# Performance work log

Hardware: AMD Instinct MI355X
Metric: run time of the kernel (lower is better)

Reference implementation:

```python
import jax, jax.numpy as jnp
import numpy as np

N = 10000       # nodes
E = 320000      # edges (avg degree 32)
F_IN = 128      # node_in_fts
F_OUT = 128     # node_out_fts
H = 4           # num_heads_node
E_IN = 64       # edge_in_fts
HOPS = 3        # nr_of_hops
SLOPE = 0.2     # LeakyReLU negative slope (GAT default)


def setup_inputs() -> dict:
    key = jax.random.key(0)
    ks = jax.random.split(key, 10)
    s = 0.05
    return {
        "node_fts": jax.random.normal(ks[0], (N, F_IN), dtype=jnp.float32),
        "edge_fts": jax.random.normal(ks[1], (E, E_IN), dtype=jnp.float32),
        "edges": jax.random.randint(ks[2], (2, E), 0, N),
        # per-hop GATConv params (all hops share dims, stacked on axis 0)
        "Ws": jax.random.normal(ks[3], (HOPS, F_IN, H * F_OUT), dtype=jnp.float32) * s,
        "Wes": jax.random.normal(ks[4], (HOPS, E_IN, H * F_OUT), dtype=jnp.float32) * s,
        "a_src": jax.random.normal(ks[5], (HOPS, H, F_OUT), dtype=jnp.float32) * s,
        "a_dst": jax.random.normal(ks[6], (HOPS, H, F_OUT), dtype=jnp.float32) * s,
        "a_edge": jax.random.normal(ks[7], (HOPS, H, F_OUT), dtype=jnp.float32) * s,
        # gated residual params
        "W_prior": jax.random.normal(ks[8], (F_OUT, F_OUT), dtype=jnp.float32) * s,
        "W_curr": jax.random.normal(ks[9], (F_OUT, F_OUT), dtype=jnp.float32) * s,
    }


def _gat_conv(x, edge_fts, src, dst, W, We, asrc, adst, aedge):
    # dense projections: [N,H,F_OUT] and [E,H,F_OUT]
    h = (x @ W).reshape(-1, H, F_OUT)
    he = (edge_fts @ We).reshape(-1, H, F_OUT)
    h_src = h[src]                                   # [E,H,F_OUT] gather
    # per-edge attention logits [E,H]
    alpha = (h_src * asrc).sum(-1) + (h[dst] * adst).sum(-1) + (he * aedge).sum(-1)
    alpha = jax.nn.leaky_relu(alpha, SLOPE)
    # segment softmax over incoming edges of each destination node
    amax = jnp.full((N, H), -jnp.inf, dtype=alpha.dtype).at[dst].max(alpha)
    w = jnp.exp(alpha - amax[dst])                   # [E,H]
    denom = jax.ops.segment_sum(w, dst, num_segments=N) + 1e-16  # [N,H]
    msg = w[:, :, None] * h_src                      # [E,H,F_OUT]
    out = jax.ops.segment_sum(msg, dst, num_segments=N) / denom[:, :, None]
    return out.mean(axis=1)                          # mean head aggregation -> [N,F_OUT]


def reference(node_fts, edge_fts, edges, Ws, Wes, a_src, a_dst, a_edge, W_prior, W_curr):
    src, dst = edges[0], edges[1]
    x = node_fts
    prior = None
    for i in range(HOPS):
        curr = _gat_conv(x, edge_fts, src, dst, Ws[i], Wes[i], a_src[i], a_dst[i], a_edge[i])
        if prior is None:
            x = curr
        else:
            gate = jax.nn.sigmoid(prior @ W_prior + curr @ W_curr)
            x = gate * curr + (1.0 - gate) * prior
        prior = x
    return x
```

## Files before the change

### kernel.cpp

```cpp
#include <hip/hip_runtime.h>
#include <hip/hip_fp16.h>

#define N_NODES 10000
#define E_EDGES 320000
#define NH 4
#define HOPS 3
#define WMAX 128

typedef _Float16 f16x8 __attribute__((ext_vector_type(8)));
typedef _Float16 f16x4 __attribute__((ext_vector_type(4)));
typedef float    f32x4 __attribute__((ext_vector_type(4)));

__global__ void k_count(const int* __restrict__ dst, int* __restrict__ counts){
  int e = blockIdx.x*256 + threadIdx.x;
  if(e < E_EDGES) atomicAdd(&counts[dst[e]], 1);
}

__global__ __launch_bounds__(1024) void k_scan(const int* __restrict__ counts,
                                               int* __restrict__ row_ptr, int* __restrict__ fillp){
  __shared__ int sm[1024];
  int t = threadIdx.x;
  const int CH = 10;
  int base = t*CH;
  int loc[CH]; int sum = 0;
  #pragma unroll
  for(int i=0;i<CH;i++){
    int v = (base+i < N_NODES) ? counts[base+i] : 0;
    loc[i] = sum; sum += v;
  }
  sm[t] = sum; __syncthreads();
  for(int off=1; off<1024; off<<=1){
    int add = (t>=off) ? sm[t-off] : 0;
    __syncthreads();
    sm[t] += add;
    __syncthreads();
  }
  int excl = (t>0) ? sm[t-1] : 0;
  #pragma unroll
  for(int i=0;i<CH;i++){
    int n = base+i;
    if(n < N_NODES){
      int e = excl + loc[i];
      row_ptr[n] = e;
      fillp[n]   = e;
    }
  }
  if(t==1023) row_ptr[N_NODES] = sm[1023];
}

__global__ void k_fill(const int* __restrict__ src, const int* __restrict__ dst,
                       int* __restrict__ fillp, int* __restrict__ csr_eid, int* __restrict__ sorted_src){
  int e = blockIdx.x*256 + threadIdx.x;
  if(e < E_EDGES){
    int d = dst[e];
    int pos = atomicAdd(&fillp[d], 1);
    csr_eid[pos] = e;
    sorted_src[pos] = src[e];
  }
}

__global__ __launch_bounds__(256) void k_setup(const float* __restrict__ node_fts, _Float16* __restrict__ xh,
                       const float* __restrict__ Ws, _Float16* __restrict__ WsT,
                       const float* __restrict__ Wes, const float* __restrict__ a_edge,
                       float* __restrict__ b_edge){
  __shared__ float lds[32][65];
  int b = blockIdx.x, t = threadIdx.x;
  if(b < 1250){
    int i = b*256 + t;
    float4 v = *(const float4*)(node_fts + (size_t)i*4);
    f16x4 h = { (_Float16)v.x, (_Float16)v.y, (_Float16)v.z, (_Float16)v.w };
    *(f16x4*)(xh + (size_t)i*4) = h;
  } else if(b < 1346){
    int b2 = b - 1250;
    int hop = b2>>5, rem = b2&31, kt = rem>>3, ct = rem&7;
    int k0 = kt*32, c0 = ct*64;
    const float* wsrc = Ws + (size_t)hop*65536;
    #pragma unroll
    for(int i=0;i<8;i++){
      int u = t + i*256;
      int kk = u>>6, cc = u&63;
      lds[kk][cc] = wsrc[(size_t)(k0+kk)*512 + c0 + cc];
    }
    __syncthreads();
    _Float16* wdst = WsT + (size_t)hop*512*128;
    #pragma unroll
    for(int i=0;i<2;i++){
      int u = t + i*256;
      int c = u>>3, kq = (u&7)*4;
      f16x4 h = { (_Float16)lds[kq][c], (_Float16)lds[kq+1][c],
                  (_Float16)lds[kq+2][c], (_Float16)lds[kq+3][c] };
      *(f16x4*)(wdst + (size_t)(c0+c)*128 + k0 + kq) = h;
    }
  } else {
    int idx = (b-1346)*256 + t;
    if(idx < HOPS*64*NH){
      int hop = idx/(64*NH); int c = (idx/NH)%64; int h = idx%NH;
      const float* we = Wes + (size_t)hop*64*512 + (size_t)c*512 + h*128;
      const float* ae = a_edge + (size_t)hop*NH*128 + h*128;
      float s = 0.f;
      for(int f=0; f<128; f++) s += we[f] * ae[f];
      b_edge[idx] = s;
    }
  }
}

__global__ __launch_bounds__(256) void k_alpha_mfma(const float* __restrict__ edge_fts,
                        const float* __restrict__ b_edge, float* __restrict__ ae_nat){
  __shared__ float tile[64][20];
  int w = threadIdx.x>>6, l = threadIdx.x&63;
  int col = l&15, kgrp = l>>4;
  f16x8 bf0, bf1;
  #pragma unroll
  for(int j=0;j<8;j++){
    int k0 = 0*32 + kgrp*8 + j;
    int k1 = 1*32 + kgrp*8 + j;
    float v0 = 0.f, v1 = 0.f;
    if(col < 12){
      int hop = col>>2, h = col&3;
      v0 = b_edge[hop*256 + k0*4 + h];
      v1 = b_edge[hop*256 + k1*4 + h];
    }
    bf0[j] = (_Float16)v0;
    bf1[j] = (_Float16)v1;
  }
  int e0 = blockIdx.x*64 + w*16;
  int erow = e0 + (l&15);
  const float* ef = edge_fts + (size_t)erow*64 + kgrp*8;
  f32x4 acc = {0.f,0.f,0.f,0.f};
  {
    float4 x0 = *(const float4*)(ef);
    float4 x1 = *(const float4*)(ef + 4);
    f16x8 a = { (_Float16)x0.x,(_Float16)x0.y,(_Float16)x0.z,(_Float16)x0.w,
                (_Float16)x1.x,(_Float16)x1.y,(_Float16)x1.z,(_Float16)x1.w };
    acc = __builtin_amdgcn_mfma_f32_16x16x32_f16(a, bf0, acc, 0, 0, 0);
  }
  {
    float4 x0 = *(const float4*)(ef + 32);
    float4 x1 = *(const float4*)(ef + 36);
    f16x8 a = { (_Float16)x0.x,(_Float16)x0.y,(_Float16)x0.z,(_Float16)x0.w,
                (_Float16)x1.x,(_Float16)x1.y,(_Float16)x1.z,(_Float16)x1.w };
    acc = __builtin_amdgcn_mfma_f32_16x16x32_f16(a, bf1, acc, 0, 0, 0);
  }
  int crow = (l>>4)*4;
  #pragma unroll
  for(int r=0;r<4;r++) tile[w*16 + crow + r][col] = acc[r];
  __syncthreads();
  int u = threadIdx.x;
  int edge = u>>2, q = u&3;
  *(float4*)(ae_nat + ((size_t)(blockIdx.x*64 + edge))*16 + q*4) = *(const float4*)&tile[edge][q*4];
}

__global__ __launch_bounds__(256) void k_projm(const _Float16* __restrict__ xh,
                       const _Float16* __restrict__ Wt, __half* __restrict__ h_all){
  __shared__ __align__(16) __half tile[64][72];
  int w = threadIdx.x>>6, l = threadIdx.x&63;
  int rowb = blockIdx.x*64;
  int row0 = rowb + w*16;
  int col0 = blockIdx.y*64;
  int ar = l&15, ac = (l>>4)*8;
  f32x4 acc0 = {0.f,0.f,0.f,0.f}, acc1 = acc0, acc2 = acc0, acc3 = acc0;
  #pragma unroll
  for(int kk=0; kk<4; kk++){
    f16x8 a  = *(const f16x8*)(xh + (size_t)(row0+ar)*128 + kk*32 + ac);
    f16x8 b0 = *(const f16x8*)(Wt + (size_t)(col0 +  0 + ar)*128 + kk*32 + ac);
    f16x8 b1 = *(const f16x8*)(Wt + (size_t)(col0 + 16 + ar)*128 + kk*32 + ac);
    f16x8 b2 = *(const f16x8*)(Wt + (size_t)(col0 + 32 + ar)*128 + kk*32 + ac);
    f16x8 b3 = *(const f16x8*)(Wt + (size_t)(col0 + 48 + ar)*128 + kk*32 + ac);
    acc0 = __builtin_amdgcn_mfma_f32_16x16x32_f16(a, b0, acc0, 0, 0, 0);
    acc1 = __builtin_amdgcn_mfma_f32_16x16x32_f16(a, b1, acc1, 0, 0, 0);
    acc2 = __builtin_amdgcn_mfma_f32_16x16x32_f16(a, b2, acc2, 0, 0, 0);
    acc3 = __builtin_amdgcn_mfma_f32_16x16x32_f16(a, b3, acc3, 0, 0, 0);
  }
  int crow = (l>>4)*4, ccol = l&15;
  #pragma unroll
  for(int r=0; r<4; r++){
    int tr = w*16 + crow + r;
    tile[tr][ccol     ] = __float2half(acc0[r]);
    tile[tr][ccol + 16] = __float2half(acc1[r]);
    tile[tr][ccol + 32] = __float2half(acc2[r]);
    tile[tr][ccol + 48] = __float2half(acc3[r]);
  }
  __syncthreads();
  #pragma unroll
  for(int i=0;i<2;i++){
    int u = threadIdx.x + i*256;
    int row = u>>3, cq = (u&7)*8;
    int grow = rowb + row;
    if(grow < N_NODES)
      *(float4*)(h_all + (size_t)grow*512 + col0 + cq) = *(const float4*)&tile[row][cq];
  }
}

__global__ __launch_bounds__(256) void k_s(const __half* __restrict__ h_all, const float* __restrict__ asrc,
                    const float* __restrict__ adst, float* __restrict__ s_src, float* __restrict__ s_dst){
  int nw = blockIdx.x*4 + (threadIdx.x>>6);
  int l = threadIdx.x&63;
  if(nw >= N_NODES) return;
  int h = l>>4, f8 = (l&15)*8;
  const __half* hp = h_all + (size_t)nw*512 + (h<<7) + f8;
  float4 raw = *(const float4*)hp;
  const __half2* hh = (const __half2*)&raw;
  float2 c0 = __half22float2(hh[0]);
  float2 c1 = __half22float2(hh[1]);
  float2 c2 = __half22float2(hh[2]);
  float2 c3 = __half22float2(hh[3]);
  float4 a0 = *(const float4*)(asrc + (h<<7) + f8);
  float4 a1 = *(const float4*)(asrc + (h<<7) + f8 + 4);
  float4 d0 = *(const float4*)(adst + (h<<7) + f8);
  float4 d1 = *(const float4*)(adst + (h<<7) + f8 + 4);
  float ps = c0.x*a0.x + c0.y*a0.y + c1.x*a0.z + c1.y*a0.w
           + c2.x*a1.x + c2.y*a1.y + c3.x*a1.z + c3.y*a1.w;
  float pd = c0.x*d0.x + c0.y*d0.y + c1.x*d0.z + c1.y*d0.w
           + c2.x*d1.x + c2.y*d1.y + c3.x*d1.z + c3.y*d1.w;
  #pragma unroll
  for(int off=1; off<16; off<<=1){ ps += __shfl_xor(ps,off); pd += __shfl_xor(pd,off); }
  if((l&15)==0){ s_src[nw*4+h] = ps; s_dst[nw*4+h] = pd; }
}

__global__ __launch_bounds__(256) void k_softagg(
    const float* __restrict__ ae_nat, int hop, const float* __restrict__ s_src,
    const float* __restrict__ s_dst, const int* __restrict__ sorted_src,
    const int* __restrict__ csr_eid, const int* __restrict__ row_ptr,
    const __half* __restrict__ h_all,
    float* __restrict__ ew_fb, float* __restrict__ xout, _Float16* __restrict__ xh)
{
  __shared__ float ws4[4][WMAX*4];
  __shared__ int   ssm4[4][WMAX];
  int wv = threadIdx.x>>6, l = threadIdx.x&63;
  int n = blockIdx.x*4 + wv;
  if(n >= N_NODES) return;
  int start = row_ptr[n], end = row_ptr[n+1];
  int deg = end - start;
  bool fits = (deg <= WMAX);
  float* ws = ws4[wv];
  int*   ssm = ssm4[wv];

  float4 sd = *(const float4*)(s_dst + (size_t)n*4);
  float m0=-1e30f, m1=-1e30f, m2=-1e30f, m3=-1e30f;
  float aR[2][4];

  if(fits){
    #pragma unroll
    for(int k=0;k<2;k++){
      int idx = l + k*64;
      if(idx < deg){
        int pos = start + idx;
        int s = sorted_src[pos];
        int e = csr_eid[pos];
        float4 ss = *(const float4*)(s_src + (size_t)s*4);
        float4 av = *(const float4*)(ae_nat + (size_t)e*16 + hop*4);
        float a0 = ss.x+sd.x+av.x; a0=(a0>0.f)?a0:0.2f*a0;
        float a1 = ss.y+sd.y+av.y; a1=(a1>0.f)?a1:0.2f*a1;
        float a2 = ss.z+sd.z+av.z; a2=(a2>0.f)?a2:0.2f*a2;
        float a3 = ss.w+sd.w+av.w; a3=(a3>0.f)?a3:0.2f*a3;
        aR[k][0]=a0; aR[k][1]=a1; aR[k][2]=a2; aR[k][3]=a3;
        ssm[idx] = s;
        m0=fmaxf(m0,a0); m1=fmaxf(m1,a1); m2=fmaxf(m2,a2); m3=fmaxf(m3,a3);
      }
    }
  } else {
    for(int pos=start+l; pos<end; pos+=64){
      int s = sorted_src[pos];
      int e = csr_eid[pos];
      float4 ss = *(const float4*)(s_src + (size_t)s*4);
      float4 av = *(const float4*)(ae_nat + (size_t)e*16 + hop*4);
      float a0 = ss.x+sd.x+av.x; a0=(a0>0.f)?a0:0.2f*a0;
      float a1 = ss.y+sd.y+av.y; a1=(a1>0.f)?a1:0.2f*a1;
      float a2 = ss.z+sd.z+av.z; a2=(a2>0.f)?a2:0.2f*a2;
      float a3 = ss.w+sd.w+av.w; a3=(a3>0.f)?a3:0.2f*a3;
      *(float4*)(ew_fb + (size_t)pos*4) = make_float4(a0,a1,a2,a3);
      m0=fmaxf(m0,a0); m1=fmaxf(m1,a1); m2=fmaxf(m2,a2); m3=fmaxf(m3,a3);
    }
  }
  #pragma unroll
  for(int off=32; off; off>>=1){
    m0=fmaxf(m0,__shfl_xor(m0,off)); m1=fmaxf(m1,__shfl_xor(m1,off));
    m2=fmaxf(m2,__shfl_xor(m2,off)); m3=fmaxf(m3,__shfl_xor(m3,off));
  }

  float s0=0.f,s1=0.f,s2=0.f,s3=0.f;
  if(fits){
    #pragma unroll
    for(int k=0;k<2;k++){
      int idx = l + k*64;
      if(idx < deg){
        float w0=__expf(aR[k][0]-m0), w1=__expf(aR[k][1]-m1);
        float w2=__expf(aR[k][2]-m2), w3=__expf(aR[k][3]-m3);
        int sl = idx*4;
        ws[sl]=w0; ws[sl+1]=w1; ws[sl+2]=w2; ws[sl+3]=w3;
        s0+=w0; s1+=w1; s2+=w2; s3+=w3;
      }
    }
  } else {
    for(int pos=start+l; pos<end; pos+=64){
      float4 a = *(const float4*)(ew_fb + (size_t)pos*4);
      float w0=__expf(a.x-m0), w1=__expf(a.y-m1), w2=__expf(a.z-m2), w3=__expf(a.w-m3);
      *(float4*)(ew_fb + (size_t)pos*4) = make_float4(w0,w1,w2,w3);
      s0+=w0; s1+=w1; s2+=w2; s3+=w3;
    }
  }
  #pragma unroll
  for(int off=32; off; off>>=1){
    s0+=__shfl_xor(s0,off); s1+=__shfl_xor(s1,off);
    s2+=__shfl_xor(s2,off); s3+=__shfl_xor(s3,off);
  }

  int h = l>>4, f8 = (l&15)*8;
  float dh = (h==0)?s0:((h==1)?s1:((h==2)?s2:s3));
  float inv = 1.f/(dh + 1e-16f);
  float acc[8] = {0.f,0.f,0.f,0.f,0.f,0.f,0.f,0.f};
  for(int sl=0; sl<deg; sl++){
    int s; float w;
    if(fits){ s = ssm[sl]; w = ws[sl*4 + h]; }
    else    { s = sorted_src[start+sl]; w = ew_fb[(size_t)(start+sl)*4 + h]; }
    const __half* hp = h_all + (size_t)s*512 + (h<<7) + f8;
    float4 raw = *(const float4*)hp;
    const __half2* hh = (const __half2*)&raw;
    float2 c0 = __half22float2(hh[0]);
    float2 c1 = __half22float2(hh[1]);
    float2 c2 = __half22float2(hh[2]);
    float2 c3 = __half22float2(hh[3]);
    acc[0]+=w*c0.x; acc[1]+=w*c0.y; acc[2]+=w*c1.x; acc[3]+=w*c1.y;
    acc[4]+=w*c2.x; acc[5]+=w*c2.y; acc[6]+=w*c3.x; acc[7]+=w*c3.y;
  }
  #pragma unroll
  for(int i=0;i<8;i++){
    acc[i] *= inv;
    acc[i] += __shfl_xor(acc[i], 16);
    acc[i] += __shfl_xor(acc[i], 32);
    acc[i] *= 0.25f;
  }
  if(l < 16){
    int f0 = l*8;
    *(float4*)(xout + (size_t)n*128 + f0)     = make_float4(acc[0],acc[1],acc[2],acc[3]);
    *(float4*)(xout + (size_t)n*128 + f0 + 4) = make_float4(acc[4],acc[5],acc[6],acc[7]);
    if(xh){
      f16x8 hv = { (_Float16)acc[0],(_Float16)acc[1],(_Float16)acc[2],(_Float16)acc[3],
                   (_Float16)acc[4],(_Float16)acc[5],(_Float16)acc[6],(_Float16)acc[7] };
      *(f16x8*)(xh + (size_t)n*128 + f0) = hv;
    }
  }
}

__global__ __launch_bounds__(256) void k_gate2(const float* __restrict__ prior, const float* __restrict__ curr,
                       const float* __restrict__ Wp, const float* __restrict__ Wc,
                       float* __restrict__ xnew, _Float16* __restrict__ xh){
  __shared__ float pr[32][132];
  __shared__ float cu[32][132];
  int t = threadIdx.x;
  int n0 = blockIdx.x*32;
  int c0 = blockIdx.y*64;
  #pragma unroll
  for(int i=0;i<4;i++){
    int u = t + i*256;
    int row = u>>5, c4 = (u&31)<<2;
    float4 v = make_float4(0.f,0.f,0.f,0.f), w = v;
    if(n0+row < N_NODES){
      v = *(const float4*)(prior + (size_t)(n0+row)*128 + c4);
      w = *(const float4*)(curr  + (size_t)(n0+row)*128 + c4);
    }
    *(float4*)&pr[row][c4] = v;
    *(float4*)&cu[row][c4] = w;
  }
  __syncthreads();
  int tc = t&15, tr = t>>4;
  int r0 = tr*2, cc = c0 + tc*4;
  float accp[2][4] = {{0.f,0.f,0.f,0.f},{0.f,0.f,0.f,0.f}};
  float accc[2][4] = {{0.f,0.f,0.f,0.f},{0.f,0.f,0.f,0.f}};
  #pragma unroll 4
  for(int k=0;k<128;k++){
    float4 wp = *(const float4*)(Wp + (size_t)k*128 + cc);
    float4 wc = *(const float4*)(Wc + (size_t)k*128 + cc);
    #pragma unroll
    for(int i=0;i<2;i++){
      float ap = pr[r0+i][k], ac = cu[r0+i][k];
      accp[i][0]+=ap*wp.x; accp[i][1]+=ap*wp.y; accp[i][2]+=ap*wp.z; accp[i][3]+=ap*wp.w;
      accc[i][0]+=ac*wc.x; accc[i][1]+=ac*wc.y; accc[i][2]+=ac*wc.z; accc[i][3]+=ac*wc.w;
    }
  }
  #pragma unroll
  for(int i=0;i<2;i++){
    int row = n0 + r0 + i;
    if(row < N_NODES){
      float oj[4];
      #pragma unroll
      for(int j=0;j<4;j++){
        float z = accp[i][j]+accc[i][j];
        float g = 1.f/(1.f+__expf(-z));
        oj[j] = g*cu[r0+i][cc + j] + (1.f-g)*pr[r0+i][cc + j];
      }
      *(float4*)(xnew + (size_t)row*128 + cc) = make_float4(oj[0],oj[1],oj[2],oj[3]);
      if(xh){
        f16x4 hv = { (_Float16)oj[0], (_Float16)oj[1], (_Float16)oj[2], (_Float16)oj[3] };
        *(f16x4*)(xh + (size_t)row*128 + cc) = hv;
      }
    }
  }
}

extern "C" void kernel_launch(void* const* d_in, const int* in_sizes, int n_in,
                              void* d_out, int out_size, void* d_ws, size_t ws_size,
                              hipStream_t stream){
  (void)in_sizes; (void)n_in; (void)out_size; (void)ws_size;
  const float* node_fts = (const float*)d_in[0];
  const float* edge_fts = (const float*)d_in[1];
  const int*   edges    = (const int*)d_in[2];
  const float* Ws       = (const float*)d_in[3];
  const float* Wes      = (const float*)d_in[4];
  const float* a_src    = (const float*)d_in[5];
  const float* a_dst    = (const float*)d_in[6];
  const float* a_edge   = (const float*)d_in[7];
  const float* W_prior  = (const float*)d_in[8];
  const float* W_curr   = (const float*)d_in[9];

  char* ws = (char*)d_ws;
  size_t off = 0;
  auto alloc = [&](size_t bytes)->void*{
    void* p = ws + off;
    off += (bytes + 255) & ~(size_t)255;
    return p;
  };
  int*       counts     = (int*)      alloc((size_t)N_NODES*4);
  int*       row_ptr    = (int*)      alloc((size_t)(N_NODES+1)*4);
  int*       fillp      = (int*)      alloc((size_t)N_NODES*4);
  int*       csr_eid    = (int*)      alloc((size_t)E_EDGES*4);
  int*       sorted_src = (int*)      alloc((size_t)E_EDGES*4);
  float*     b_edge     = (float*)    alloc((size_t)HOPS*64*NH*4);
  float*     ae_nat     = (float*)    alloc((size_t)E_EDGES*16*4);
  __half*    h_all      = (__half*)   alloc((size_t)N_NODES*512*2);
  float*     s_src      = (float*)    alloc((size_t)N_NODES*NH*4);
  float*     s_dst      = (float*)    alloc((size_t)N_NODES*NH*4);
  float*     ew_fb      = (float*)    alloc((size_t)E_EDGES*NH*4);
  float*     xbuf       = (float*)    alloc((size_t)N_NODES*128*4);
  float*     curbuf     = (float*)    alloc((size_t)N_NODES*128*4);
  _Float16*  xh         = (_Float16*) alloc((size_t)10112*128*2);
  _Float16*  WsT        = (_Float16*) alloc((size_t)HOPS*512*128*2);

  const int* src = edges;
  const int* dst = edges + E_EDGES;

  (void)hipMemsetAsync(counts, 0, (size_t)N_NODES*4, stream);
  k_count<<<(E_EDGES+255)/256, 256, 0, stream>>>(dst, counts);
  k_scan<<<1, 1024, 0, stream>>>(counts, row_ptr, fillp);
  k_fill<<<(E_EDGES+255)/256, 256, 0, stream>>>(src, dst, fillp, csr_eid, sorted_src);
  k_setup<<<1349, 256, 0, stream>>>(node_fts, xh, Ws, WsT, Wes, a_edge, b_edge);
  k_alpha_mfma<<<5000, 256, 0, stream>>>(edge_fts, b_edge, ae_nat);

  for(int hop=0; hop<HOPS; hop++){
    k_projm<<<dim3(157, 8), 256, 0, stream>>>(xh, WsT + (size_t)hop*512*128, h_all);
    k_s<<<2500, 256, 0, stream>>>(h_all, a_src + (size_t)hop*512, a_dst + (size_t)hop*512, s_src, s_dst);
    float* xout = (hop==0) ? xbuf : curbuf;
    k_softagg<<<2500, 256, 0, stream>>>(ae_nat, hop, s_src, s_dst,
                                        sorted_src, csr_eid, row_ptr, h_all, ew_fb, xout,
                                        (hop==0) ? xh : (_Float16*)nullptr);
    if(hop > 0){
      float* xnew = (hop == HOPS-1) ? (float*)d_out : xbuf;
      k_gate2<<<dim3(313, 2), 256, 0, stream>>>(xbuf, curbuf, W_prior, W_curr, xnew,
                                                (hop < HOPS-1) ? xh : (_Float16*)nullptr);
    }
  }
}
```

Measured before the change: 345.8 us.

## Store edge attention terms in CSR order per hop and unroll aggregation by four

The edge-term kernel now gathers edge feature rows through csr_eid and writes its results in destination-sorted order, in a separate contiguous array for each hop. The softmax/aggregation kernel can then read them with coalesced loads by CSR position, with no csr_eid indirection. The weighted neighbour-feature accumulation is also unrolled four ways with independent accumulators so more gathers are in flight at once. The cost is moved to a one-time gather of edge_fts rows in the setup kernel, plus higher register pressure in the aggregation kernel.

```diff
diff --git a/kernel.cpp b/kernel.cpp
--- a/kernel.cpp
+++ b/kernel.cpp
@@ -105,7 +105,8 @@
 }
 
 __global__ __launch_bounds__(256) void k_alpha_mfma(const float* __restrict__ edge_fts,
-                        const float* __restrict__ b_edge, float* __restrict__ ae_nat){
+                        const int* __restrict__ csr_eid, const float* __restrict__ b_edge,
+                        float* __restrict__ ae_sorted){
   __shared__ float tile[64][20];
   int w = threadIdx.x>>6, l = threadIdx.x&63;
   int col = l&15, kgrp = l>>4;
@@ -123,8 +124,8 @@
     bf0[j] = (_Float16)v0;
     bf1[j] = (_Float16)v1;
   }
-  int e0 = blockIdx.x*64 + w*16;
-  int erow = e0 + (l&15);
+  int pos0 = blockIdx.x*64 + w*16;
+  int erow = csr_eid[pos0 + (l&15)];
   const float* ef = edge_fts + (size_t)erow*64 + kgrp*8;
   f32x4 acc = {0.f,0.f,0.f,0.f};
   {
@@ -147,7 +148,10 @@
   __syncthreads();
   int u = threadIdx.x;
   int edge = u>>2, q = u&3;
-  *(float4*)(ae_nat + ((size_t)(blockIdx.x*64 + edge))*16 + q*4) = *(const float4*)&tile[edge][q*4];
+  if(q < 3){
+    *(float4*)(ae_sorted + (size_t)q*E_EDGES*4 + ((size_t)(blockIdx.x*64 + edge))*4)
+      = *(const float4*)&tile[edge][q*4];
+  }
 }
 
 __global__ __launch_bounds__(256) void k_projm(const _Float16* __restrict__ xh,
@@ -218,10 +222,9 @@
 }
 
 __global__ __launch_bounds__(256) void k_softagg(
-    const float* __restrict__ ae_nat, int hop, const float* __restrict__ s_src,
+    const float* __restrict__ ae, const float* __restrict__ s_src,
     const float* __restrict__ s_dst, const int* __restrict__ sorted_src,
-    const int* __restrict__ csr_eid, const int* __restrict__ row_ptr,
-    const __half* __restrict__ h_all,
+    const int* __restrict__ row_ptr, const __half* __restrict__ h_all,
     float* __restrict__ ew_fb, float* __restrict__ xout, _Float16* __restrict__ xh)
 {
   __shared__ float ws4[4][WMAX*4];
@@ -246,9 +249,8 @@
       if(idx < deg){
         int pos = start + idx;
         int s = sorted_src[pos];
-        int e = csr_eid[pos];
         float4 ss = *(const float4*)(s_src + (size_t)s*4);
-        float4 av = *(const float4*)(ae_nat + (size_t)e*16 + hop*4);
+        float4 av = *(const float4*)(ae + (size_t)pos*4);
         float a0 = ss.x+sd.x+av.x; a0=(a0>0.f)?a0:0.2f*a0;
         float a1 = ss.y+sd.y+av.y; a1=(a1>0.f)?a1:0.2f*a1;
         float a2 = ss.z+sd.z+av.z; a2=(a2>0.f)?a2:0.2f*a2;
@@ -261,9 +263,8 @@
   } else {
     for(int pos=start+l; pos<end; pos+=64){
       int s = sorted_src[pos];
-      int e = csr_eid[pos];
       float4 ss = *(const float4*)(s_src + (size_t)s*4);
-      float4 av = *(const float4*)(ae_nat + (size_t)e*16 + hop*4);
+      float4 av = *(const float4*)(ae + (size_t)pos*4);
       float a0 = ss.x+sd.x+av.x; a0=(a0>0.f)?a0:0.2f*a0;
       float a1 = ss.y+sd.y+av.y; a1=(a1>0.f)?a1:0.2f*a1;
       float a2 = ss.z+sd.z+av.z; a2=(a2>0.f)?a2:0.2f*a2;
@@ -308,23 +309,60 @@
   int h = l>>4, f8 = (l&15)*8;
   float dh = (h==0)?s0:((h==1)?s1:((h==2)?s2:s3));
   float inv = 1.f/(dh + 1e-16f);
-  float acc[8] = {0.f,0.f,0.f,0.f,0.f,0.f,0.f,0.f};
-  for(int sl=0; sl<deg; sl++){
-    int s; float w;
-    if(fits){ s = ssm[sl]; w = ws[sl*4 + h]; }
-    else    { s = sorted_src[start+sl]; w = ew_fb[(size_t)(start+sl)*4 + h]; }
-    const __half* hp = h_all + (size_t)s*512 + (h<<7) + f8;
-    float4 raw = *(const float4*)hp;
-    const __half2* hh = (const __half2*)&raw;
-    float2 c0 = __half22float2(hh[0]);
-    float2 c1 = __half22float2(hh[1]);
-    float2 c2 = __half22float2(hh[2]);
-    float2 c3 = __half22float2(hh[3]);
-    acc[0]+=w*c0.x; acc[1]+=w*c0.y; acc[2]+=w*c1.x; acc[3]+=w*c1.y;
-    acc[4]+=w*c2.x; acc[5]+=w*c2.y; acc[6]+=w*c3.x; acc[7]+=w*c3.y;
-  }
+  float ac0[8]={0,0,0,0,0,0,0,0}, ac1[8]={0,0,0,0,0,0,0,0};
+  float ac2[8]={0,0,0,0,0,0,0,0}, ac3[8]={0,0,0,0,0,0,0,0};
+  int hoff = (h<<7) + f8;
+  int sl = 0;
+  if(fits){
+    for(; sl+4 <= deg; sl+=4){
+      int sA = ssm[sl], sB = ssm[sl+1], sC = ssm[sl+2], sD = ssm[sl+3];
+      float wA = ws[sl*4+h], wB = ws[(sl+1)*4+h], wC = ws[(sl+2)*4+h], wD = ws[(sl+3)*4+h];
+      float4 rA = *(const float4*)(h_all + (size_t)sA*512 + hoff);
+      float4 rB = *(const float4*)(h_all + (size_t)sB*512 + hoff);
+      float4 rC = *(const float4*)(h_all + (size_t)sC*512 + hoff);
+      float4 rD = *(const float4*)(h_all + (size_t)sD*512 + hoff);
+      const __half2* hA = (const __half2*)&rA;
+      const __half2* hB = (const __half2*)&rB;
+      const __half2* hC = (const __half2*)&rC;
+      const __half2* hD = (const __half2*)&rD;
+      #pragma unroll
+      for(int j=0;j<4;j++){
+        float2 vA = __half22float2(hA[j]);
+        float2 vB = __half22float2(hB[j]);
+        float2 vC = __half22float2(hC[j]);
+        float2 vD = __half22float2(hD[j]);
+        ac0[2*j]+=wA*vA.x; ac0[2*j+1]+=wA*vA.y;
+        ac1[2*j]+=wB*vB.x; ac1[2*j+1]+=wB*vB.y;
+        ac2[2*j]+=wC*vC.x; ac2[2*j+1]+=wC*vC.y;
+        ac3[2*j]+=wD*vD.x; ac3[2*j+1]+=wD*vD.y;
+      }
+    }
+    for(; sl < deg; sl++){
+      int s = ssm[sl]; float w = ws[sl*4+h];
+      float4 r = *(const float4*)(h_all + (size_t)s*512 + hoff);
+      const __half2* hh = (const __half2*)&r;
+      #pragma unroll
+      for(int j=0;j<4;j++){
+        float2 v = __half22float2(hh[j]);
+        ac0[2*j]+=w*v.x; ac0[2*j+1]+=w*v.y;
+      }
+    }
+  } else {
+    for(; sl < deg; sl++){
+      int s = sorted_src[start+sl]; float w = ew_fb[(size_t)(start+sl)*4+h];
+      float4 r = *(const float4*)(h_all + (size_t)s*512 + hoff);
+      const __half2* hh = (const __half2*)&r;
+      #pragma unroll
+      for(int j=0;j<4;j++){
+        float2 v = __half22float2(hh[j]);
+        ac0[2*j]+=w*v.x; ac0[2*j+1]+=w*v.y;
+      }
+    }
+  }
+  float acc[8];
   #pragma unroll
   for(int i=0;i<8;i++){
+    acc[i] = (ac0[i]+ac1[i]) + (ac2[i]+ac3[i]);
     acc[i] *= inv;
     acc[i] += __shfl_xor(acc[i], 16);
     acc[i] += __shfl_xor(acc[i], 32);
@@ -426,7 +464,7 @@
   int*       csr_eid    = (int*)      alloc((size_t)E_EDGES*4);
   int*       sorted_src = (int*)      alloc((size_t)E_EDGES*4);
   float*     b_edge     = (float*)    alloc((size_t)HOPS*64*NH*4);
-  float*     ae_nat     = (float*)    alloc((size_t)E_EDGES*16*4);
+  float*     ae_sorted  = (float*)    alloc((size_t)HOPS*E_EDGES*NH*4);
   __half*    h_all      = (__half*)   alloc((size_t)N_NODES*512*2);
   float*     s_src      = (float*)    alloc((size_t)N_NODES*NH*4);
   float*     s_dst      = (float*)    alloc((size_t)N_NODES*NH*4);
@@ -444,14 +482,14 @@
   k_scan<<<1, 1024, 0, stream>>>(counts, row_ptr, fillp);
   k_fill<<<(E_EDGES+255)/256, 256, 0, stream>>>(src, dst, fillp, csr_eid, sorted_src);
   k_setup<<<1349, 256, 0, stream>>>(node_fts, xh, Ws, WsT, Wes, a_edge, b_edge);
-  k_alpha_mfma<<<5000, 256, 0, stream>>>(edge_fts, b_edge, ae_nat);
+  k_alpha_mfma<<<5000, 256, 0, stream>>>(edge_fts, csr_eid, b_edge, ae_sorted);
 
   for(int hop=0; hop<HOPS; hop++){
     k_projm<<<dim3(157, 8), 256, 0, stream>>>(xh, WsT + (size_t)hop*512*128, h_all);
     k_s<<<2500, 256, 0, stream>>>(h_all, a_src + (size_t)hop*512, a_dst + (size_t)hop*512, s_src, s_dst);
     float* xout = (hop==0) ? xbuf : curbuf;
-    k_softagg<<<2500, 256, 0, stream>>>(ae_nat, hop, s_src, s_dst,
-                                        sorted_src, csr_eid, row_ptr, h_all, ew_fb, xout,
+    k_softagg<<<2500, 256, 0, stream>>>(ae_sorted + (size_t)hop*E_EDGES*4, s_src, s_dst,
+                                        sorted_src, row_ptr, h_all, ew_fb, xout,
                                         (hop==0) ? xh : (_Float16*)nullptr);
     if(hop > 0){
       float* xnew = (hop == HOPS-1) ? (float*)d_out : xbuf;
```

Result: faster. 315.3 us (-8.8%).
